# Kernel optimization log

Measured on AMD Instinct MI355X. Metric: run time of the kernel, lower is better.

## Reference

```python
import jax, jax.numpy as jnp
import numpy as np

B, C, N, S, DCONV = 16, 128, 2000, 8, 4
DI = 2 * N            # mamba expand=2
DT_RANK = (N + 15) // 16


def setup_inputs() -> dict:
    key = jax.random.key(0)
    ks = jax.random.split(key, 10)
    r = lambda k, sh, s=0.02: jax.random.normal(k, sh, jnp.float32) * s
    return {
        "x": jax.random.normal(ks[0], (B, C, N, 1), jnp.float32),
        "bn1_g": jnp.ones((C,), jnp.float32), "bn1_b": jnp.zeros((C,), jnp.float32),
        "conv1_w": r(ks[1], (C, C)), "conv1_b": jnp.zeros((C,), jnp.float32),
        "ln_w": jnp.ones((N,), jnp.float32), "ln_b": jnp.zeros((N,), jnp.float32),
        "W_in": r(ks[2], (2 * DI, N)),
        "convm_w": r(ks[3], (DI, DCONV), 0.1), "convm_b": jnp.zeros((DI,), jnp.float32),
        "W_x": r(ks[4], (DT_RANK + 2 * S, DI)),
        "W_dt": r(ks[5], (DI, DT_RANK), 0.1), "b_dt": jnp.full((DI,), -2.0, jnp.float32),
        "A_log": jnp.log(jnp.broadcast_to(jnp.arange(1, S + 1, dtype=jnp.float32), (DI, S))),
        "D_p": jnp.ones((DI,), jnp.float32),
        "W_out": r(ks[6], (N, DI)),
        "bn3_g": jnp.ones((C,), jnp.float32), "bn3_b": jnp.zeros((C,), jnp.float32),
        "conv3_w": r(ks[7], (C, C)), "conv3_b": jnp.zeros((C,), jnp.float32),
    }


def _inorm(x, eps=1e-3):
    # InstanceNorm2d (no affine): per-sample, per-channel over spatial dims
    m = x.mean(axis=(2, 3), keepdims=True)
    v = x.var(axis=(2, 3), keepdims=True)
    return (x - m) * jax.lax.rsqrt(v + eps)


def _bnorm(x, g, b, eps=1e-5):
    # BatchNorm2d (training-mode stats) over (B, H, W) per channel
    m = x.mean(axis=(0, 2, 3), keepdims=True)
    v = x.var(axis=(0, 2, 3), keepdims=True)
    return (x - m) * jax.lax.rsqrt(v + eps) * g[None, :, None, None] + b[None, :, None, None]


def _block(x, g, b, w, cb):
    # InstanceNorm -> BatchNorm -> ReLU -> 1x1 Conv2d
    h = jax.nn.relu(_bnorm(_inorm(x), g, b))
    return jnp.einsum('bcnw,oc->bonw', h, w) + cb[None, :, None, None]


def _mamba(u, W_in, cw, cb, W_x, W_dt, b_dt, A_log, D_p, W_out):
    # u: [B, L, D] with L=C (seq), D=N (d_model)
    L = u.shape[1]
    xz = jnp.einsum('bld,ed->ble', u, W_in)          # [B,L,2*DI]
    xi, z = jnp.split(xz, 2, axis=-1)
    # depthwise causal conv1d along L (d_conv=4)
    xp = jnp.pad(xi, ((0, 0), (DCONV - 1, 0), (0, 0)))
    xc = sum(xp[:, k:k + L, :] * cw[:, k] for k in range(DCONV)) + cb
    xc = jax.nn.silu(xc)                             # [B,L,DI]
    xdbl = jnp.einsum('bld,ed->ble', xc, W_x)        # [B,L,dt_rank+2S]
    dt = jax.nn.softplus(jnp.einsum('blr,dr->bld', xdbl[..., :DT_RANK], W_dt) + b_dt)
    Bm = xdbl[..., DT_RANK:DT_RANK + S]              # [B,L,S]
    Cm = xdbl[..., DT_RANK + S:]                     # [B,L,S]
    A = -jnp.exp(A_log)                              # [DI,S]

    def step(h, inp):
        dt_l, B_l, C_l, u_l = inp                    # [B,DI],[B,S],[B,S],[B,DI]
        dA = jnp.exp(dt_l[..., None] * A)            # [B,DI,S]
        h = dA * h + (dt_l * u_l)[..., None] * B_l[:, None, :]
        return h, jnp.einsum('bds,bs->bd', h, C_l)

    seq = (jnp.swapaxes(dt, 0, 1), jnp.swapaxes(Bm, 0, 1),
           jnp.swapaxes(Cm, 0, 1), jnp.swapaxes(xc, 0, 1))
    h0 = jnp.zeros((u.shape[0], DI, S), u.dtype)
    _, ys = jax.lax.scan(step, h0, seq)              # ys: [L,B,DI]
    y = jnp.swapaxes(ys, 0, 1) + xc * D_p
    y = y * jax.nn.silu(z)
    return jnp.einsum('ble,de->bld', y, W_out)       # [B,L,D]


def reference(x, bn1_g, bn1_b, conv1_w, conv1_b, ln_w, ln_b, W_in, convm_w,
              convm_b, W_x, W_dt, b_dt, A_log, D_p, W_out, bn3_g, bn3_b,
              conv3_w, conv3_b):
    out = _block(x, bn1_g, bn1_b, conv1_w, conv1_b)[..., 0]   # [B,C,N]
    mu = out.mean(-1, keepdims=True)
    var = out.var(-1, keepdims=True)
    out_n = (out - mu) * jax.lax.rsqrt(var + 1e-5) * ln_w + ln_b  # LayerNorm(points)
    out = out + _mamba(out_n, W_in, convm_w, convm_b, W_x, W_dt, b_dt, A_log, D_p, W_out)
    out = _block(out[..., None], bn3_g, bn3_b, conv3_w, conv3_b)  # [B,C,N,1]
    return out + x
```

## Files before the change

### kernel.cpp

```cpp
#include <hip/hip_runtime.h>
#include <cmath>
#include <cstdint>

#define Bc   16
#define Cc   128
#define Nc   2000
#define Lc   128
#define DIc  4000
#define Sc   8
#define RKc  125
#define E2c  8000
#define EXc  141

#define KP1  2016
#define NP1  8064

__device__ __forceinline__ unsigned short f2bf(float f) {
  union { float f; unsigned int u; } v; v.f = f;
  unsigned int r = v.u + 0x7FFFu + ((v.u >> 16) & 1u);
  return (unsigned short)(r >> 16);
}

__global__ void inorm_stats(const float* __restrict__ in,
                            float* __restrict__ mout,
                            float* __restrict__ vout) {
  int bc = blockIdx.x;
  const float* p = in + (long)bc * Nc;
  float s = 0.f, sq = 0.f;
  for (int i = threadIdx.x; i < Nc; i += blockDim.x) {
    float x = p[i]; s += x; sq += x * x;
  }
  #pragma unroll
  for (int o = 32; o > 0; o >>= 1) {
    s  += __shfl_down(s, o, 64);
    sq += __shfl_down(sq, o, 64);
  }
  __shared__ float ss[4], sqq[4];
  int w = threadIdx.x >> 6, lane = threadIdx.x & 63;
  if (lane == 0) { ss[w] = s; sqq[w] = sq; }
  __syncthreads();
  if (threadIdx.x == 0) {
    s  = ss[0] + ss[1] + ss[2] + ss[3];
    sq = sqq[0] + sqq[1] + sqq[2] + sqq[3];
    float mean = s / Nc;
    float var  = sq / Nc - mean * mean;
    mout[bc] = mean; vout[bc] = var;
  }
}

__global__ void bn_scale(const float* __restrict__ v, float* __restrict__ bnsc) {
  int c = threadIdx.x;
  if (c >= Cc) return;
  float s = 0.f;
  for (int b = 0; b < Bc; b++) {
    float vv = v[b * Cc + c];
    s += vv / (vv + 1e-3f);
  }
  bnsc[c] = rsqrtf(s / Bc + 1e-5f);
}

__global__ void compute_h_t(const float* __restrict__ in,
                            const float* __restrict__ m,
                            const float* __restrict__ v,
                            const float* __restrict__ bnsc,
                            const float* __restrict__ g,
                            const float* __restrict__ bb,
                            unsigned short* __restrict__ hT) {
  int b  = blockIdx.y;
  int n0 = blockIdx.x * 64;
  __shared__ unsigned short tile[64][132];
  int t  = threadIdx.x;
  int nl = t & 63, cb = t >> 6;
  int n  = n0 + nl;
  #pragma unroll 4
  for (int p = 0; p < 32; p++) {
    int c = p * 4 + cb;
    float val = 0.f;
    if (n < Nc) {
      int bc = b * Cc + c;
      float xn = (in[(long)bc * Nc + n] - m[bc]) * rsqrtf(v[bc] + 1e-3f);
      val = fmaxf(xn * bnsc[c] * g[c] + bb[c], 0.f);
    }
    tile[nl][c] = f2bf(val);
  }
  __syncthreads();
  int r = t >> 2, c0 = (t & 3) * 32;
  int nr = n0 + r;
  if (nr < Nc) {
    unsigned int* dst = (unsigned int*)(hT + ((long)b * 2048 + nr) * 128 + c0);
    const unsigned short* src = &tile[r][c0];
    #pragma unroll
    for (int j = 0; j < 16; j++)
      dst[j] = *(const unsigned int*)(src + 2 * j);
  }
}

__global__ void reduce_slices(const float* __restrict__ sl, float* __restrict__ dst,
                              long stride, int ns, int total, int accum) {
  int i = blockIdx.x * 256 + threadIdx.x;
  if (i >= total) return;
  float s = accum ? dst[i] : 0.f;
  for (int k = 0; k < ns; k++) s += sl[(long)k * stride + i];
  dst[i] = s;
}

__global__ void reduce_xdbl(const float* __restrict__ sl,
                            float* __restrict__ xd,
                            unsigned short* __restrict__ xdb) {
  int i = blockIdx.x * 256 + threadIdx.x;
  if (i >= 2048 * 144) return;
  int row = i / 144, c = i - row * 144;
  float s = 0.f;
  if (c < EXc) {
    #pragma unroll
    for (int k = 0; k < 4; k++) s += sl[(long)k * (2048 * 256) + (long)row * 256 + c];
    xd[(long)row * EXc + c] = s;
  }
  if (c < 128) xdb[(long)row * 128 + c] = f2bf(c < RKc ? s : 0.f);
}

__global__ void cvt_pad_bf16(const float* __restrict__ src, unsigned short* __restrict__ dst,
                             int R, int Cdst, int Rsrc, int Csrc) {
  long i = (long)blockIdx.x * 256 + threadIdx.x;
  long total = (long)R * Cdst;
  if (i >= total) return;
  int r = (int)(i / Cdst), c = (int)(i - (long)r * Cdst);
  float v = (r < Rsrc && c < Csrc) ? src[(long)r * Csrc + c] : 0.f;
  dst[i] = f2bf(v);
}

__global__ void ln_rows(const float* __restrict__ in,
                        const float* __restrict__ lw,
                        const float* __restrict__ lb,
                        unsigned short* __restrict__ An) {
  int row = blockIdx.x;
  const float* p = in + (long)row * Nc;
  float s = 0.f, sq = 0.f;
  for (int i = threadIdx.x; i < Nc; i += blockDim.x) {
    float x = p[i]; s += x; sq += x * x;
  }
  #pragma unroll
  for (int o = 32; o > 0; o >>= 1) {
    s  += __shfl_down(s, o, 64);
    sq += __shfl_down(sq, o, 64);
  }
  __shared__ float ss[4], sqq[4];
  __shared__ float smean, srstd;
  int w = threadIdx.x >> 6, lane = threadIdx.x & 63;
  if (lane == 0) { ss[w] = s; sqq[w] = sq; }
  __syncthreads();
  if (threadIdx.x == 0) {
    s  = ss[0] + ss[1] + ss[2] + ss[3];
    sq = sqq[0] + sqq[1] + sqq[2] + sqq[3];
    float mean = s / Nc;
    float var  = sq / Nc - mean * mean;
    smean = mean; srstd = rsqrtf(var + 1e-5f);
  }
  __syncthreads();
  float mu = smean, rs = srstd;
  for (int i = threadIdx.x; i < KP1; i += blockDim.x) {
    float v = 0.f;
    if (i < Nc) v = (p[i] - mu) * rs * lw[i] + lb[i];
    An[(long)row * KP1 + i] = f2bf(v);
  }
}

typedef short v8s __attribute__((ext_vector_type(8)));
typedef float v4f __attribute__((ext_vector_type(4)));

typedef const __attribute__((address_space(1))) unsigned int* as1_cu32p;
typedef __attribute__((address_space(3))) unsigned int* as3_u32p;

__device__ __forceinline__ void gload_lds16(const unsigned short* g, unsigned short* l) {
  __builtin_amdgcn_global_load_lds((as1_cu32p)(uintptr_t)g,
                                   (as3_u32p)(uintptr_t)l, 16, 0, 0);
}

__global__ __launch_bounds__(256, 4)
void gemm_mfma_bt(const unsigned short* __restrict__ A,
                  const unsigned short* __restrict__ B,
                  float* C, int NN, int K, int lda, int ldb, int ldc,
                  long sA, long sB, long sC,
                  int KS, int Klen, long sliceStride,
                  int epi, const float* __restrict__ ebias,
                  const float* __restrict__ addp) {
  __shared__ unsigned short As[128 * 32];
  __shared__ unsigned short Bs[128 * 32];

  int z = blockIdx.z;
  int batch = z / KS, ks = z - batch * KS;
  const unsigned short* Ab = A + (long)batch * sA;
  const unsigned short* Bb = B + (long)batch * sB;
  float* Cs = C + (long)batch * sC + (long)ks * sliceStride;
  const float* X = addp ? addp + (long)batch * sC : nullptr;

  int k0 = ks * Klen;
  int kend = min(K, k0 + Klen);

  int i0 = blockIdx.y * 128;
  int j0 = blockIdx.x * 128;

  int t = threadIdx.x;
  int wave = t >> 6, lane = t & 63;
  int wm = wave >> 1, wn = wave & 1;

  int srow = lane >> 2;
  int scol = lane & 3;
  const unsigned short* gA0 = Ab + (long)(i0 + wave * 32 + srow) * lda + scol * 8;
  const unsigned short* gA1 = gA0 + (long)16 * lda;
  const unsigned short* gB0 = Bb + (long)(j0 + wave * 32 + srow) * ldb + scol * 8;
  const unsigned short* gB1 = gB0 + (long)16 * ldb;
  unsigned short* lA0 = As + (wave * 32) * 32;
  unsigned short* lA1 = As + (wave * 32 + 16) * 32;
  unsigned short* lB0 = Bs + (wave * 32) * 32;
  unsigned short* lB1 = Bs + (wave * 32 + 16) * 32;

  int fr = lane & 15;
  int kq = lane >> 4;

  v4f acc[4][4] = {};

  for (int kt = k0; kt < kend; kt += 32) {
    gload_lds16(gA0 + kt, lA0);
    gload_lds16(gA1 + kt, lA1);
    gload_lds16(gB0 + kt, lB0);
    gload_lds16(gB1 + kt, lB1);
    __syncthreads();

    v8s af[4], bfr[4];
    #pragma unroll
    for (int mt = 0; mt < 4; mt++)
      af[mt] = *(const v8s*)&As[(wm * 64 + mt * 16 + fr) * 32 + kq * 8];
    #pragma unroll
    for (int nt = 0; nt < 4; nt++)
      bfr[nt] = *(const v8s*)&Bs[(wn * 64 + nt * 16 + fr) * 32 + kq * 8];

    #pragma unroll
    for (int mt = 0; mt < 4; mt++)
      #pragma unroll
      for (int nt = 0; nt < 4; nt++)
        acc[mt][nt] = __builtin_amdgcn_mfma_f32_16x16x32_bf16(
            af[mt], bfr[nt], acc[mt][nt], 0, 0, 0);
    __syncthreads();
  }

  int orow = (lane >> 4) * 4;
  int ocol = lane & 15;
  #pragma unroll
  for (int mt = 0; mt < 4; mt++) {
    #pragma unroll
    for (int nt = 0; nt < 4; nt++) {
      int gi = i0 + wm * 64 + mt * 16 + orow;
      int gj = j0 + wn * 64 + nt * 16 + ocol;
      if (gj >= NN) continue;
      #pragma unroll
      for (int r = 0; r < 4; r++) {
        long idx = (long)(gi + r) * ldc + gj;
        float v = acc[mt][nt][r];
        if (epi == 1) {
          float tr = v + ebias[gj];
          v = fmaxf(tr, 0.f) + log1pf(__expf(-fabsf(tr)));
        } else if (epi == 2) {
          if (gj >= DIc) v = v / (1.f + __expf(-v));
        } else if (epi == 3) {
          v += ebias[gi + r];
          if (X) v += X[idx];
        }
        Cs[idx] = v;
      }
    }
  }
}

__global__ void dwconv_silu(const float* __restrict__ xz,
                            const float4* __restrict__ cw,
                            const float* __restrict__ cb,
                            float* __restrict__ xc,
                            unsigned short* __restrict__ xcb, int total) {
  int i = blockIdx.x * 256 + threadIdx.x;
  if (i >= total) return;
  int d  = i % DIc;
  int bl = i / DIc;
  int l  = bl % Lc;
  int b  = bl / Lc;
  float4 w = cw[d];
  float acc = cb[d];
  long rowbase = (long)(b * Lc) * E2c + d;
  int l0 = l - 3;
  if (l0     >= 0) acc += xz[rowbase + (long)l0       * E2c] * w.x;
  if (l0 + 1 >= 0) acc += xz[rowbase + (long)(l0 + 1) * E2c] * w.y;
  if (l0 + 2 >= 0) acc += xz[rowbase + (long)(l0 + 2) * E2c] * w.z;
  acc += xz[rowbase + (long)l * E2c] * w.w;
  float sv = acc / (1.f + __expf(-acc));
  xc[i] = sv;
  xcb[i] = f2bf(sv);
}

#define SCU 4
__global__ __launch_bounds__(256)
void scan_kernel(const float* __restrict__ dtv,
                 const float* __restrict__ xdbl,
                 const float* __restrict__ xc,
                 const float* __restrict__ xzf,
                 const float* __restrict__ A_log,
                 const float* __restrict__ D_p,
                 unsigned short* __restrict__ yb) {
  int d = blockIdx.x * 256 + threadIdx.x;
  int b = blockIdx.y;
  if (d >= DIc) return;
  float Av[Sc];
  #pragma unroll
  for (int s = 0; s < Sc; s++) Av[s] = -__expf(A_log[d * Sc + s]);
  float Dp = D_p[d];
  float h[Sc];
  #pragma unroll
  for (int s = 0; s < Sc; s++) h[s] = 0.f;

  long base  = (long)(b * Lc) * DIc + d;
  long zbase = (long)(b * Lc) * E2c + DIc + d;
  const float* xrow = xdbl + (long)(b * Lc) * EXc + RKc;

  float d0[SCU], u0[SCU], z0[SCU], B0[SCU][Sc], C0[SCU][Sc];
  float d1[SCU], u1[SCU], z1[SCU], B1[SCU][Sc], C1[SCU][Sc];

#define LOADG(g, dd, uu, zz, BB, CC)                                        \
  { int l0_ = (g) * SCU;                                                    \
    _Pragma("unroll")                                                       \
    for (int u = 0; u < SCU; u++) {                                         \
      long idx = base + (long)(l0_ + u) * DIc;                              \
      dd[u] = dtv[idx];                                                     \
      uu[u] = xc[idx];                                                      \
      zz[u] = xzf[zbase + (long)(l0_ + u) * E2c];                           \
      const float* xr = xrow + (long)(l0_ + u) * EXc;                       \
      _Pragma("unroll")                                                     \
      for (int s = 0; s < Sc; s++) { BB[u][s] = xr[s]; CC[u][s] = xr[Sc + s]; } \
    } }

#define COMPG(g, dd, uu, zz, BB, CC)                                        \
  { int l0_ = (g) * SCU;                                                    \
    _Pragma("unroll")                                                       \
    for (int u = 0; u < SCU; u++) {                                         \
      float dv = dd[u], uv = uu[u];                                         \
      float du = dv * uv;                                                   \
      float p = 0.f;                                                        \
      _Pragma("unroll")                                                     \
      for (int s = 0; s < Sc; s++) {                                        \
        float dA = __expf(dv * Av[s]);                                      \
        h[s] = dA * h[s] + du * BB[u][s];                                   \
        p += h[s] * CC[u][s];                                               \
      }                                                                     \
      yb[base + (long)(l0_ + u) * DIc] = f2bf((p + uv * Dp) * zz[u]);       \
    } }

  LOADG(0, d0, u0, z0, B0, C0);
  #pragma unroll 1
  for (int g = 0; g < Lc / SCU; g += 2) {
    LOADG(g + 1, d1, u1, z1, B1, C1);
    COMPG(g, d0, u0, z0, B0, C0);
    if (g + 2 < Lc / SCU) LOADG(g + 2, d0, u0, z0, B0, C0);
    COMPG(g + 1, d1, u1, z1, B1, C1);
  }
#undef LOADG
#undef COMPG
}

extern "C" void kernel_launch(void* const* d_in, const int* in_sizes, int n_in,
                              void* d_out, int out_size, void* d_ws, size_t ws_size,
                              hipStream_t stream) {
  const float* x       = (const float*)d_in[0];
  const float* bn1_g   = (const float*)d_in[1];
  const float* bn1_b   = (const float*)d_in[2];
  const float* conv1_w = (const float*)d_in[3];
  const float* conv1_b = (const float*)d_in[4];
  const float* ln_w    = (const float*)d_in[5];
  const float* ln_b    = (const float*)d_in[6];
  const float* W_in    = (const float*)d_in[7];
  const float* convm_w = (const float*)d_in[8];
  const float* convm_b = (const float*)d_in[9];
  const float* W_x     = (const float*)d_in[10];
  const float* W_dt    = (const float*)d_in[11];
  const float* b_dt    = (const float*)d_in[12];
  const float* A_log   = (const float*)d_in[13];
  const float* D_p     = (const float*)d_in[14];
  const float* W_out   = (const float*)d_in[15];
  const float* bn3_g   = (const float*)d_in[16];
  const float* bn3_b   = (const float*)d_in[17];
  const float* conv3_w = (const float*)d_in[18];
  const float* conv3_b = (const float*)d_in[19];
  float* out = (float*)d_out;
  float* ws  = (float*)d_ws;

  const int TOT  = Bc * Cc * Nc;
  const int ROWS = Bc * Lc;

  float* m1    = ws;
  float* v1    = ws + 2048;
  float* bnsc  = ws + 4096;
  float* h     = ws + 8192;
  float* out1  = h    + (long)TOT;
  float* outn  = out1 + (long)TOT;
  float* xz    = outn + (long)TOT;
  float* xc    = xz   + (long)ROWS * E2c;
  float* xdbl  = xc   + (long)ROWS * DIc;
  float* dtb   = xdbl + (long)ROWS * EXc;

  unsigned short* An      = (unsigned short*)outn;
  unsigned short* Bwin    = (unsigned short*)dtb;
  unsigned short* Bwx     = (unsigned short*)outn;
  unsigned short* Bwdt    = (unsigned short*)(outn + 512000);
  float*          xdbl_sl = outn + 800000;
  unsigned short* xdbl_b  = (unsigned short*)(outn + 2900000);
  unsigned short* W1b     = (unsigned short*)(outn + 3100000);
  unsigned short* W3b     = (unsigned short*)(outn + 3200000);
  unsigned short* hT      = (unsigned short*)h;
  unsigned short* xcb     = (unsigned short*)h;
  unsigned short* Bwout   = (unsigned short*)h;
  unsigned short* yb      = (unsigned short*)out;
  float*          wout_sl = xz;

  dim3 b256(256);
  int gElem = (TOT + 255) / 256;

  inorm_stats<<<dim3(Bc * Cc), b256, 0, stream>>>(x, m1, v1);
  bn_scale<<<dim3(1), dim3(128), 0, stream>>>(v1, bnsc);
  compute_h_t<<<dim3(32, Bc), b256, 0, stream>>>(x, m1, v1, bnsc, bn1_g, bn1_b, hT);
  cvt_pad_bf16<<<dim3(64), b256, 0, stream>>>(conv1_w, W1b, 128, 128, Cc, Cc);
  {
    dim3 g(16, 1, Bc);
    gemm_mfma_bt<<<g, b256, 0, stream>>>(W1b, hT, out1, Nc, 128, 128, 128, Nc,
                                         0L, 2048L * 128, (long)Cc * Nc,
                                         1, 128, 0L, 3, conv1_b, nullptr);
  }

  ln_rows<<<dim3(ROWS), b256, 0, stream>>>(out1, ln_w, ln_b, An);

  {
    long tot = (long)NP1 * KP1;
    cvt_pad_bf16<<<dim3((unsigned)((tot + 255) / 256)), b256, 0, stream>>>(
        W_in, Bwin, NP1, KP1, E2c, Nc);
  }

  {
    dim3 g(NP1 / 128, ROWS / 128, 1);
    gemm_mfma_bt<<<g, b256, 0, stream>>>(An, Bwin, xz, E2c, KP1, KP1, KP1, E2c,
                                         0L, 0L, 0L, 1, KP1, 0L, 2, nullptr, nullptr);
  }

  cvt_pad_bf16<<<dim3((256 * 4000 + 255) / 256), b256, 0, stream>>>(
      W_x, Bwx, 256, 4000, EXc, DIc);
  cvt_pad_bf16<<<dim3((4096 * 128 + 255) / 256), b256, 0, stream>>>(
      W_dt, Bwdt, 4096, 128, DIc, RKc);

  {
    int tot = ROWS * DIc;
    dwconv_silu<<<dim3((tot + 255) / 256), b256, 0, stream>>>(
        xz, (const float4*)convm_w, convm_b, xc, xcb, tot);
  }

  {
    dim3 g(2, ROWS / 128, 4);
    gemm_mfma_bt<<<g, b256, 0, stream>>>(xcb, Bwx, xdbl_sl, 256, DIc,
                                         DIc, DIc, 256, 0L, 0L, 0L,
                                         4, 1024, 2048L * 256, 0, nullptr, nullptr);
    int tot = 2048 * 144;
    reduce_xdbl<<<dim3((tot + 255) / 256), b256, 0, stream>>>(xdbl_sl, xdbl, xdbl_b);
  }

  {
    dim3 g(4096 / 128, ROWS / 128, 1);
    gemm_mfma_bt<<<g, b256, 0, stream>>>(xdbl_b, Bwdt, dtb, DIc, 128,
                                         128, 128, DIc, 0L, 0L, 0L,
                                         1, 128, 0L, 1, b_dt, nullptr);
  }

  {
    long tot = (long)2048 * DIc;
    cvt_pad_bf16<<<dim3((unsigned)((tot + 255) / 256)), b256, 0, stream>>>(
        W_out, Bwout, 2048, DIc, Nc, DIc);
  }

  scan_kernel<<<dim3((DIc + 255) / 256, Bc), b256, 0, stream>>>(
      dtb, xdbl, xc, xz, A_log, D_p, yb);

  {
    dim3 g(2048 / 128, ROWS / 128, 2);
    gemm_mfma_bt<<<g, b256, 0, stream>>>(yb, Bwout, wout_sl, Nc, DIc, DIc, DIc, Nc,
                                         0L, 0L, 0L, 2, 2048, (long)TOT,
                                         0, nullptr, nullptr);
    reduce_slices<<<dim3(gElem), b256, 0, stream>>>(
        wout_sl, out1, (long)TOT, 2, TOT, 1);
  }

  inorm_stats<<<dim3(Bc * Cc), b256, 0, stream>>>(out1, m1, v1);
  bn_scale<<<dim3(1), dim3(128), 0, stream>>>(v1, bnsc);
  compute_h_t<<<dim3(32, Bc), b256, 0, stream>>>(out1, m1, v1, bnsc, bn3_g, bn3_b, hT);
  cvt_pad_bf16<<<dim3(64), b256, 0, stream>>>(conv3_w, W3b, 128, 128, Cc, Cc);
  {
    dim3 g(16, 1, Bc);
    gemm_mfma_bt<<<g, b256, 0, stream>>>(W3b, hT, out, Nc, 128, 128, 128, Nc,
                                         0L, 2048L * 128, (long)Cc * Nc,
                                         1, 128, 0L, 3, conv3_b, x);
  }
}
```

Before: 666.7 us.

## Store in_proj output as bf16 and remap GEMM blocks for L2 locality

The in_proj GEMM now writes its xz output in bf16 instead of fp32. The depthwise conv and scan kernels read it back through a bf16-to-float helper, roughly halving the traffic for this large intermediate. The in_proj and out_proj GEMMs also switch to a 1D launch with a custom block-to-tile mapping that groups tiles by row and column, aiming for better L2 reuse of operands. The cost is bf16 rounding on the x and z branches, which adds some numerical error.

```diff
diff --git a/kernel.cpp b/kernel.cpp
--- a/kernel.cpp
+++ b/kernel.cpp
@@ -19,6 +19,9 @@
   union { float f; unsigned int u; } v; v.f = f;
   unsigned int r = v.u + 0x7FFFu + ((v.u >> 16) & 1u);
   return (unsigned short)(r >> 16);
+}
+__device__ __forceinline__ float bf2f(unsigned short u) {
+  union { unsigned int i; float f; } v; v.i = ((unsigned int)u) << 16; return v.f;
 }
 
 __global__ void inorm_stats(const float* __restrict__ in,
@@ -183,12 +186,32 @@
                   long sA, long sB, long sC,
                   int KS, int Klen, long sliceStride,
                   int epi, const float* __restrict__ ebias,
-                  const float* __restrict__ addp) {
+                  const float* __restrict__ addp,
+                  int mode, int jret, int obf) {
   __shared__ unsigned short As[128 * 32];
   __shared__ unsigned short Bs[128 * 32];
 
-  int z = blockIdx.z;
-  int batch = z / KS, ks = z - batch * KS;
+  int i0, j0, ks = 0, batch = 0;
+  if (mode == 1) {
+    int L = blockIdx.x;
+    int q = L & 7, w = L >> 3;
+    i0 = (w & 15) * 128;
+    int jg = w >> 4;
+    j0 = (jg * 8 + q) * 128;
+    if (j0 >= jret) return;
+  } else if (mode == 2) {
+    int L = blockIdx.x;
+    int q = L & 7, w = L >> 3;
+    i0 = (w & 15) * 128;
+    int r = w >> 4;
+    ks = r >> 1;
+    j0 = (q * 2 + (r & 1)) * 128;
+  } else {
+    int z = blockIdx.z;
+    batch = z / KS; ks = z - batch * KS;
+    i0 = blockIdx.y * 128; j0 = blockIdx.x * 128;
+  }
+
   const unsigned short* Ab = A + (long)batch * sA;
   const unsigned short* Bb = B + (long)batch * sB;
   float* Cs = C + (long)batch * sC + (long)ks * sliceStride;
@@ -196,9 +219,6 @@
 
   int k0 = ks * Klen;
   int kend = min(K, k0 + Klen);
-
-  int i0 = blockIdx.y * 128;
-  int j0 = blockIdx.x * 128;
 
   int t = threadIdx.x;
   int wave = t >> 6, lane = t & 63;
@@ -266,13 +286,14 @@
           v += ebias[gi + r];
           if (X) v += X[idx];
         }
-        Cs[idx] = v;
+        if (obf) ((unsigned short*)Cs)[idx] = f2bf(v);
+        else Cs[idx] = v;
       }
     }
   }
 }
 
-__global__ void dwconv_silu(const float* __restrict__ xz,
+__global__ void dwconv_silu(const unsigned short* __restrict__ xzb,
                             const float4* __restrict__ cw,
                             const float* __restrict__ cb,
                             float* __restrict__ xc,
@@ -287,10 +308,10 @@
   float acc = cb[d];
   long rowbase = (long)(b * Lc) * E2c + d;
   int l0 = l - 3;
-  if (l0     >= 0) acc += xz[rowbase + (long)l0       * E2c] * w.x;
-  if (l0 + 1 >= 0) acc += xz[rowbase + (long)(l0 + 1) * E2c] * w.y;
-  if (l0 + 2 >= 0) acc += xz[rowbase + (long)(l0 + 2) * E2c] * w.z;
-  acc += xz[rowbase + (long)l * E2c] * w.w;
+  if (l0     >= 0) acc += bf2f(xzb[rowbase + (long)l0       * E2c]) * w.x;
+  if (l0 + 1 >= 0) acc += bf2f(xzb[rowbase + (long)(l0 + 1) * E2c]) * w.y;
+  if (l0 + 2 >= 0) acc += bf2f(xzb[rowbase + (long)(l0 + 2) * E2c]) * w.z;
+  acc += bf2f(xzb[rowbase + (long)l * E2c]) * w.w;
   float sv = acc / (1.f + __expf(-acc));
   xc[i] = sv;
   xcb[i] = f2bf(sv);
@@ -301,7 +322,7 @@
 void scan_kernel(const float* __restrict__ dtv,
                  const float* __restrict__ xdbl,
                  const float* __restrict__ xc,
-                 const float* __restrict__ xzf,
+                 const unsigned short* __restrict__ xzb,
                  const float* __restrict__ A_log,
                  const float* __restrict__ D_p,
                  unsigned short* __restrict__ yb) {
@@ -330,7 +351,7 @@
       long idx = base + (long)(l0_ + u) * DIc;                              \
       dd[u] = dtv[idx];                                                     \
       uu[u] = xc[idx];                                                      \
-      zz[u] = xzf[zbase + (long)(l0_ + u) * E2c];                           \
+      zz[u] = bf2f(xzb[zbase + (long)(l0_ + u) * E2c]);                     \
       const float* xr = xrow + (long)(l0_ + u) * EXc;                       \
       _Pragma("unroll")                                                     \
       for (int s = 0; s < Sc; s++) { BB[u][s] = xr[s]; CC[u][s] = xr[Sc + s]; } \
@@ -415,6 +436,7 @@
   unsigned short* hT      = (unsigned short*)h;
   unsigned short* xcb     = (unsigned short*)h;
   unsigned short* Bwout   = (unsigned short*)h;
+  unsigned short* xzb     = (unsigned short*)xz;
   unsigned short* yb      = (unsigned short*)out;
   float*          wout_sl = xz;
 
@@ -429,7 +451,7 @@
     dim3 g(16, 1, Bc);
     gemm_mfma_bt<<<g, b256, 0, stream>>>(W1b, hT, out1, Nc, 128, 128, 128, Nc,
                                          0L, 2048L * 128, (long)Cc * Nc,
-                                         1, 128, 0L, 3, conv1_b, nullptr);
+                                         1, 128, 0L, 3, conv1_b, nullptr, 0, 0, 0);
   }
 
   ln_rows<<<dim3(ROWS), b256, 0, stream>>>(out1, ln_w, ln_b, An);
@@ -441,9 +463,9 @@
   }
 
   {
-    dim3 g(NP1 / 128, ROWS / 128, 1);
-    gemm_mfma_bt<<<g, b256, 0, stream>>>(An, Bwin, xz, E2c, KP1, KP1, KP1, E2c,
-                                         0L, 0L, 0L, 1, KP1, 0L, 2, nullptr, nullptr);
+    gemm_mfma_bt<<<dim3(1024), b256, 0, stream>>>(
+        An, Bwin, (float*)xzb, E2c, KP1, KP1, KP1, E2c,
+        0L, 0L, 0L, 1, KP1, 0L, 2, nullptr, nullptr, 1, NP1, 1);
   }
 
   cvt_pad_bf16<<<dim3((256 * 4000 + 255) / 256), b256, 0, stream>>>(
@@ -454,14 +476,15 @@
   {
     int tot = ROWS * DIc;
     dwconv_silu<<<dim3((tot + 255) / 256), b256, 0, stream>>>(
-        xz, (const float4*)convm_w, convm_b, xc, xcb, tot);
+        xzb, (const float4*)convm_w, convm_b, xc, xcb, tot);
   }
 
   {
     dim3 g(2, ROWS / 128, 4);
     gemm_mfma_bt<<<g, b256, 0, stream>>>(xcb, Bwx, xdbl_sl, 256, DIc,
                                          DIc, DIc, 256, 0L, 0L, 0L,
-                                         4, 1024, 2048L * 256, 0, nullptr, nullptr);
+                                         4, 1024, 2048L * 256, 0, nullptr, nullptr,
+                                         0, 0, 0);
     int tot = 2048 * 144;
     reduce_xdbl<<<dim3((tot + 255) / 256), b256, 0, stream>>>(xdbl_sl, xdbl, xdbl_b);
   }
@@ -470,7 +493,7 @@
     dim3 g(4096 / 128, ROWS / 128, 1);
     gemm_mfma_bt<<<g, b256, 0, stream>>>(xdbl_b, Bwdt, dtb, DIc, 128,
                                          128, 128, DIc, 0L, 0L, 0L,
-                                         1, 128, 0L, 1, b_dt, nullptr);
+                                         1, 128, 0L, 1, b_dt, nullptr, 0, 0, 0);
   }
 
   {
@@ -480,13 +503,12 @@
   }
 
   scan_kernel<<<dim3((DIc + 255) / 256, Bc), b256, 0, stream>>>(
-      dtb, xdbl, xc, xz, A_log, D_p, yb);
-
-  {
-    dim3 g(2048 / 128, ROWS / 128, 2);
-    gemm_mfma_bt<<<g, b256, 0, stream>>>(yb, Bwout, wout_sl, Nc, DIc, DIc, DIc, Nc,
-                                         0L, 0L, 0L, 2, 2048, (long)TOT,
-                                         0, nullptr, nullptr);
+      dtb, xdbl, xc, xzb, A_log, D_p, yb);
+
+  {
+    gemm_mfma_bt<<<dim3(512), b256, 0, stream>>>(
+        yb, Bwout, wout_sl, Nc, DIc, DIc, DIc, Nc,
+        0L, 0L, 0L, 2, 2048, (long)TOT, 0, nullptr, nullptr, 2, 0, 0);
     reduce_slices<<<dim3(gElem), b256, 0, stream>>>(
         wout_sl, out1, (long)TOT, 2, TOT, 1);
   }
@@ -499,6 +521,6 @@
     dim3 g(16, 1, Bc);
     gemm_mfma_bt<<<g, b256, 0, stream>>>(W3b, hT, out, Nc, 128, 128, 128, Nc,
                                          0L, 2048L * 128, (long)Cc * Nc,
-                                         1, 128, 0L, 3, conv3_b, x);
-  }
-}
+                                         1, 128, 0L, 3, conv3_b, x, 0, 0, 0);
+  }
+}
```

Result: slower. 726.6 us (+9.0%).
